# Optimization experiments

Measured on AMD Instinct MI355X. Metric: run time of the kernel, lower is better.

The kernel has to match this reference:

```python
import jax, jax.numpy as jnp
import numpy as np

K = 501   # box-filter length (conv kernel height)
P = 250   # reflect padding on each side of the time axis


def setup_inputs() -> dict:
    key = jax.random.key(0)
    k1, k2 = jax.random.split(key)
    pred = jax.random.normal(k1, (8, 16384, 128), dtype=jnp.float32)  # [B, T, C]
    # Conv2d default bias init: U(-b, b) with b = 1/sqrt(fan_in) = 1/sqrt(501)
    b = 1.0 / np.sqrt(K)
    bias = jax.random.uniform(k2, (1,), dtype=jnp.float32, minval=-b, maxval=b)
    return {"pred": pred, "bias": bias}


def reference(pred, bias):
    # Reflect-pad the time axis, then compute the 501-wide moving sum via a
    # prefix-sum (O(N) instead of O(N*K) dense conv) — same math as the
    # all-ones Conv2d kernel with reflect padding.
    x = jnp.pad(pred, ((0, 0), (P, P), (0, 0)), mode="reflect")  # [B, T+2P, C]
    c = jnp.cumsum(x, axis=1)
    c = jnp.concatenate([jnp.zeros_like(c[:, :1, :]), c], axis=1)  # [B, T+2P+1, C]
    win_sum = c[:, K:, :] - c[:, :-K, :]                            # [B, T, C]
    smoothed = (win_sum + bias[0]) / K  # conv output (ones weights + bias) / kernel_size
    return jnp.maximum(pred, smoothed)
```

## Files before the change

### kernel.cpp

```cpp
#include <hip/hip_runtime.h>


constexpr int B     = 8;
constexpr int T     = 16384;
constexpr int C     = 128;
constexpr int K     = 501;
constexpr int CHN   = 32;
constexpr int NCG   = C / CHN;
constexpr int NSEG  = 32;
constexpr int SEGR  = T / NSEG;

__device__ __forceinline__ int ridx(int j) {
    j = (j < 0) ? -j : j;
    return (j >= T) ? (2 * T - 2 - j) : j;
}

__device__ __forceinline__ float scan64(float x) {
    x += __int_as_float(__builtin_amdgcn_update_dpp(
        0, __float_as_int(x), 0x111, 0xf, 0xf, true));
    x += __int_as_float(__builtin_amdgcn_update_dpp(
        0, __float_as_int(x), 0x112, 0xf, 0xf, true));
    x += __int_as_float(__builtin_amdgcn_update_dpp(
        0, __float_as_int(x), 0x114, 0xf, 0xf, true));
    x += __int_as_float(__builtin_amdgcn_update_dpp(
        0, __float_as_int(x), 0x118, 0xf, 0xf, true));
    x += __int_as_float(__builtin_amdgcn_update_dpp(
        0, __float_as_int(x), 0x142, 0xa, 0xf, false));
    x += __int_as_float(__builtin_amdgcn_update_dpp(
        0, __float_as_int(x), 0x143, 0xc, 0xf, false));
    return x;
}

__device__ __forceinline__ float bperm(int bidx, float v) {
    return __int_as_float(__builtin_amdgcn_ds_bpermute(bidx, __float_as_int(v)));
}
__device__ __forceinline__ float rl63(float x) {
    return __int_as_float(__builtin_amdgcn_readlane(__float_as_int(x), 63));
}

__global__ __launch_bounds__(512, 2) void smoother_kernel(
    const float* __restrict__ pred, const float* __restrict__ bias,
    float* __restrict__ out) {
    const int b   = blockIdx.x & 7;
    const int cg  = (blockIdx.x >> 3) & (NCG - 1);
    const int seg = blockIdx.x >> 5;
    const int g0  = seg * SEGR;

    const int tid  = threadIdx.x;
    const int lane = tid & 63;
    const int w    = tid >> 6;

    const float* pb = pred + (size_t)b * T * C + cg * CHN;
    float*       ob = out  + (size_t)b * T * C + cg * CHN;

    const float rk  = 1.0f / (float)K;
    const float brk = bias[0] * rk;

    const bool interior = (seg >= 1) && (seg <= NSEG - 2);

    const bool m5  = (lane < 5);
    const bool m11 = (lane < 11);
    const int vcidx = ((lane + 5)  & 63) << 2;
    const int voidx = ((lane + 11) & 63) << 2;

    float4 R0, R1, R2, R3, R4, R5, R6, R7, R8, R9, R10, R11, R12, R13, R14, R15;

#define LOADR(Rm, m) do {                                                   \
        const int r0_ = g0 + 64 * (m) - 261 + lane;                         \
        const int r_  = interior ? r0_ : ridx(r0_);                         \
        Rm = *reinterpret_cast<const float4*>(pb + (size_t)r_ * C + w * 4); \
    } while (0)

    LOADR(R0, 0); LOADR(R1, 1); LOADR(R2, 2); LOADR(R3, 3); LOADR(R4, 4);
    LOADR(R5, 5); LOADR(R6, 6); LOADR(R7, 7); LOADR(R8, 8);

    float4 S;
    {
        float ax = R1.x + R2.x + R3.x + R4.x + R5.x + R6.x + R7.x;
        float ay = R1.y + R2.y + R3.y + R4.y + R5.y + R6.y + R7.y;
        float az = R1.z + R2.z + R3.z + R4.z + R5.z + R6.z + R7.z;
        float aw = R1.w + R2.w + R3.w + R4.w + R5.w + R6.w + R7.w;
        if (lane >= 11) { ax += R0.x; ay += R0.y; az += R0.z; aw += R0.w; }
        #pragma unroll
        for (int dd = 1; dd <= 32; dd <<= 1) {
            ax += __shfl_xor(ax, dd);
            ay += __shfl_xor(ay, dd);
            az += __shfl_xor(az, dd);
            aw += __shfl_xor(aw, dd);
        }
        S.x = ax; S.y = ay; S.z = az; S.w = aw;
    }

#define STEP(i, RAo, RBo, RAv, RBv, RVn) do {                               \
        float4 vo_, vc_, d_, x_;                                            \
        vo_.x = bperm(voidx, m11 ? RBo.x : RAo.x);                          \
        vo_.y = bperm(voidx, m11 ? RBo.y : RAo.y);                          \
        vo_.z = bperm(voidx, m11 ? RBo.z : RAo.z);                          \
        vo_.w = bperm(voidx, m11 ? RBo.w : RAo.w);                          \
        vc_.x = bperm(vcidx, m5 ? RBv.x : RAv.x);                           \
        vc_.y = bperm(vcidx, m5 ? RBv.y : RAv.y);                           \
        vc_.z = bperm(vcidx, m5 ? RBv.z : RAv.z);                           \
        vc_.w = bperm(vcidx, m5 ? RBv.w : RAv.w);                           \
        d_.x = RVn.x - vo_.x; d_.y = RVn.y - vo_.y;                         \
        d_.z = RVn.z - vo_.z; d_.w = RVn.w - vo_.w;                         \
        x_.x = scan64(d_.x);  x_.y = scan64(d_.y);                          \
        x_.z = scan64(d_.z);  x_.w = scan64(d_.w);                          \
        float4 o_;                                                          \
        o_.x = fmaxf(vc_.x, fmaf(S.x + (x_.x - d_.x), rk, brk));            \
        o_.y = fmaxf(vc_.y, fmaf(S.y + (x_.y - d_.y), rk, brk));            \
        o_.z = fmaxf(vc_.z, fmaf(S.z + (x_.z - d_.z), rk, brk));            \
        o_.w = fmaxf(vc_.w, fmaf(S.w + (x_.w - d_.w), rk, brk));            \
        *reinterpret_cast<float4*>(                                         \
            ob + (size_t)(g0 + 64 * (i) + lane) * C + w * 4) = o_;          \
        S.x += rl63(x_.x); S.y += rl63(x_.y);                               \
        S.z += rl63(x_.z); S.w += rl63(x_.w);                               \
    } while (0)

    LOADR(R9,  9);  STEP(0, R0, R1, R4,  R5,  R8);
    LOADR(R10, 10); STEP(1, R1, R2, R5,  R6,  R9);
    LOADR(R11, 11); STEP(2, R2, R3, R6,  R7,  R10);
    LOADR(R12, 12); STEP(3, R3, R4, R7,  R8,  R11);
    LOADR(R13, 13); STEP(4, R4, R5, R8,  R9,  R12);
    LOADR(R14, 14); STEP(5, R5, R6, R9,  R10, R13);
    LOADR(R15, 15); STEP(6, R6, R7, R10, R11, R14);
                    STEP(7, R7, R8, R11, R12, R15);

#undef STEP
#undef LOADR
}

extern "C" void kernel_launch(void* const* d_in, const int* in_sizes, int n_in,
                              void* d_out, int out_size, void* d_ws, size_t ws_size,
                              hipStream_t stream) {
    const float* pred = (const float*)d_in[0];
    const float* bias = (const float*)d_in[1];
    float*       out  = (float*)d_out;

    const int blocks = B * NCG * NSEG;
    smoother_kernel<<<blocks, 512, 0, stream>>>(pred, bias, out);
}
```

Measured before the change: 156.4 us.

## Stage outputs through LDS for coalesced nontemporal stores and front-load all loads

Each step's outputs are written to a double-buffered shared-memory tile, then after a block barrier each thread stores a transposed row segment with a nontemporal store, so the global writes become contiguous per row. All 16 input loads are issued up front behind a scheduling barrier instead of being interleaved with compute. The initial wave reduction now uses the DPP scan plus a lane-63 readlane in place of xor shuffles. The cost is eight extra __syncthreads, LDS traffic, and higher register pressure from holding every load at once.

```diff
diff --git a/kernel.cpp b/kernel.cpp
--- a/kernel.cpp
+++ b/kernel.cpp
@@ -14,6 +14,8 @@
     j = (j < 0) ? -j : j;
     return (j >= T) ? (2 * T - 2 - j) : j;
 }
+
+typedef float f32x4 __attribute__((ext_vector_type(4)));
 
 __device__ __forceinline__ float scan64(float x) {
     x += __int_as_float(__builtin_amdgcn_update_dpp(
@@ -41,6 +43,8 @@
 __global__ __launch_bounds__(512, 2) void smoother_kernel(
     const float* __restrict__ pred, const float* __restrict__ bias,
     float* __restrict__ out) {
+    __shared__ __align__(16) float obuf[2][64][36];
+
     const int b   = blockIdx.x & 7;
     const int cg  = (blockIdx.x >> 3) & (NCG - 1);
     const int seg = blockIdx.x >> 5;
@@ -49,6 +53,9 @@
     const int tid  = threadIdx.x;
     const int lane = tid & 63;
     const int w    = tid >> 6;
+
+    const int srow = tid >> 3;
+    const int sq   = tid & 7;
 
     const float* pb = pred + (size_t)b * T * C + cg * CHN;
     float*       ob = out  + (size_t)b * T * C + cg * CHN;
@@ -71,8 +78,11 @@
         Rm = *reinterpret_cast<const float4*>(pb + (size_t)r_ * C + w * 4); \
     } while (0)
 
-    LOADR(R0, 0); LOADR(R1, 1); LOADR(R2, 2); LOADR(R3, 3); LOADR(R4, 4);
-    LOADR(R5, 5); LOADR(R6, 6); LOADR(R7, 7); LOADR(R8, 8);
+    LOADR(R0,  0);  LOADR(R1,  1);  LOADR(R2,  2);  LOADR(R3,  3);
+    LOADR(R4,  4);  LOADR(R5,  5);  LOADR(R6,  6);  LOADR(R7,  7);
+    LOADR(R8,  8);  LOADR(R9,  9);  LOADR(R10, 10); LOADR(R11, 11);
+    LOADR(R12, 12); LOADR(R13, 13); LOADR(R14, 14); LOADR(R15, 15);
+    __builtin_amdgcn_sched_barrier(0);
 
     float4 S;
     {
@@ -81,14 +91,10 @@
         float az = R1.z + R2.z + R3.z + R4.z + R5.z + R6.z + R7.z;
         float aw = R1.w + R2.w + R3.w + R4.w + R5.w + R6.w + R7.w;
         if (lane >= 11) { ax += R0.x; ay += R0.y; az += R0.z; aw += R0.w; }
-        #pragma unroll
-        for (int dd = 1; dd <= 32; dd <<= 1) {
-            ax += __shfl_xor(ax, dd);
-            ay += __shfl_xor(ay, dd);
-            az += __shfl_xor(az, dd);
-            aw += __shfl_xor(aw, dd);
-        }
-        S.x = ax; S.y = ay; S.z = az; S.w = aw;
+        S.x = rl63(scan64(ax));
+        S.y = rl63(scan64(ay));
+        S.z = rl63(scan64(az));
+        S.w = rl63(scan64(aw));
     }
 
 #define STEP(i, RAo, RBo, RAv, RBv, RVn) do {                               \
@@ -110,20 +116,28 @@
         o_.y = fmaxf(vc_.y, fmaf(S.y + (x_.y - d_.y), rk, brk));            \
         o_.z = fmaxf(vc_.z, fmaf(S.z + (x_.z - d_.z), rk, brk));            \
         o_.w = fmaxf(vc_.w, fmaf(S.w + (x_.w - d_.w), rk, brk));            \
-        *reinterpret_cast<float4*>(                                         \
-            ob + (size_t)(g0 + 64 * (i) + lane) * C + w * 4) = o_;          \
         S.x += rl63(x_.x); S.y += rl63(x_.y);                               \
         S.z += rl63(x_.z); S.w += rl63(x_.w);                               \
+        \
+        \
+        *reinterpret_cast<float4*>(&obuf[(i) & 1][lane][w * 4]) = o_;       \
+        __syncthreads();                                                    \
+        const float4 ov_ = *reinterpret_cast<const float4*>(                \
+            &obuf[(i) & 1][srow][sq * 4]);                                  \
+        __builtin_nontemporal_store(                                        \
+            *reinterpret_cast<const f32x4*>(&ov_),                          \
+            reinterpret_cast<f32x4*>(                                       \
+                ob + (size_t)(g0 + 64 * (i) + srow) * C + sq * 4));         \
     } while (0)
 
-    LOADR(R9,  9);  STEP(0, R0, R1, R4,  R5,  R8);
-    LOADR(R10, 10); STEP(1, R1, R2, R5,  R6,  R9);
-    LOADR(R11, 11); STEP(2, R2, R3, R6,  R7,  R10);
-    LOADR(R12, 12); STEP(3, R3, R4, R7,  R8,  R11);
-    LOADR(R13, 13); STEP(4, R4, R5, R8,  R9,  R12);
-    LOADR(R14, 14); STEP(5, R5, R6, R9,  R10, R13);
-    LOADR(R15, 15); STEP(6, R6, R7, R10, R11, R14);
-                    STEP(7, R7, R8, R11, R12, R15);
+    STEP(0, R0, R1, R4,  R5,  R8);
+    STEP(1, R1, R2, R5,  R6,  R9);
+    STEP(2, R2, R3, R6,  R7,  R10);
+    STEP(3, R3, R4, R7,  R8,  R11);
+    STEP(4, R4, R5, R8,  R9,  R12);
+    STEP(5, R5, R6, R9,  R10, R13);
+    STEP(6, R6, R7, R10, R11, R14);
+    STEP(7, R7, R8, R11, R12, R15);
 
 #undef STEP
 #undef LOADR
```

Measured after the change: 128.6 us. -17.8%, faster.
